# Performance work log

Hardware: AMD Instinct MI355X
Metric: run time of the kernel (lower is better)

## Reference

```python
import jax, jax.numpy as jnp
import numpy as np

N_ENTITY = 100000
N_RELATION = 32
DIM = 64
N_LAYER = 2
B = 4096
T = 64


def setup_inputs() -> dict:
    key = jax.random.key(0)
    ks = jax.random.split(key, 12)
    inp = {
        "items": jax.random.randint(ks[0], (B,), 0, N_ENTITY),
        "user_h": jax.random.randint(ks[1], (N_LAYER, B, T), 0, N_ENTITY),
        "user_r": jax.random.randint(ks[2], (N_LAYER, B, T), 0, N_RELATION),
        "user_t": jax.random.randint(ks[3], (N_LAYER, B, T), 0, N_ENTITY),
        "item_h": jax.random.randint(ks[4], (N_LAYER, B, T), 0, N_ENTITY),
        "item_r": jax.random.randint(ks[5], (N_LAYER, B, T), 0, N_RELATION),
        "item_t": jax.random.randint(ks[6], (N_LAYER, B, T), 0, N_ENTITY),
        # parameters (xavier-ish scale)
        "entity_emb": jax.random.normal(ks[7], (N_ENTITY, DIM), jnp.float32) * 0.05,
        "relation_emb": jax.random.normal(ks[8], (N_RELATION, DIM), jnp.float32) * 0.05,
        # torch Linear(in,out,bias=False) stored here as [in, out] so y = x @ W
        "W1": jax.random.normal(ks[9], (2 * DIM, DIM), jnp.float32) * 0.1,
        "W2": jax.random.normal(ks[10], (DIM, DIM), jnp.float32) * 0.1,
        "W3": jax.random.normal(ks[11], (DIM, 1), jnp.float32) * 0.1,
    }
    return inp


def reference(items, user_h, user_r, user_t, item_h, item_r, item_t,
              entity_emb, relation_emb, W1, W2, W3):
    def knowledge_attention(h_idx, r_idx, t_idx):
        h = entity_emb[h_idx]        # [B, T, d]
        r = relation_emb[r_idx]      # [B, T, d]
        t = entity_emb[t_idx]        # [B, T, d]
        x = jnp.concatenate([h, r], axis=-1)           # [B, T, 2d]
        a = jax.nn.relu(x @ W1)                        # [B, T, d]
        a = jax.nn.relu(a @ W2)                        # [B, T, d]
        a = jax.nn.sigmoid(jnp.squeeze(a @ W3, -1))    # [B, T]
        w = jax.nn.softmax(a, axis=-1)                 # softmax over triples
        return jnp.sum(w[..., None] * t, axis=1)       # [B, d]

    # user embeddings: origin = mean of hop-0 heads, then attention per layer; agg='sum'
    e_u = jnp.mean(entity_emb[user_h[0]], axis=1)
    for i in range(N_LAYER):
        e_u = e_u + knowledge_attention(user_h[i], user_r[i], user_t[i])

    # item embeddings: origin = item entity emb, attention per layer,
    # plus (agg=='sum', n_layer>0) extra mean of hop-0 heads
    e_v = entity_emb[items]
    for i in range(N_LAYER):
        e_v = e_v + knowledge_attention(item_h[i], item_r[i], item_t[i])
    e_v = e_v + jnp.mean(entity_emb[item_h[0]], axis=1)

    scores = jax.nn.sigmoid(jnp.sum(e_v * e_u, axis=1))  # [B]
    return scores
```

## Files before the change

kernel.cpp:

```cpp
#include <hip/hip_runtime.h>
#include <hip/hip_bf16.h>
#include <cstdint>

#define DEV static __device__ __forceinline__

typedef float        v4f __attribute__((ext_vector_type(4)));
typedef short        v8s __attribute__((ext_vector_type(8)));
typedef unsigned int v4u __attribute__((ext_vector_type(4)));

static constexpr int N_ENT = 100000;
static constexpr int BATCH = 4096;

DEV unsigned short f2bf(float f) {
    unsigned int u = __float_as_uint(f);
    u += 0x7fffu + ((u >> 16) & 1u);
    return (unsigned short)(u >> 16);
}
DEV float bflo(unsigned int w) { return __uint_as_float(w << 16); }
DEV float bfhi(unsigned int w) { return __uint_as_float(w & 0xffff0000u); }

__global__ void k0_prep(const float* __restrict__ rel, const float* __restrict__ W1,
                        const float* __restrict__ W2,
                        unsigned short* __restrict__ R1b, unsigned short* __restrict__ W2p,
                        unsigned short* __restrict__ W1p)
{
    const int gid = blockIdx.x * 256 + threadIdx.x;
    if (gid < 2048) {
        const int r = gid >> 6, j = gid & 63;
        float acc = 0.f;
        #pragma unroll 8
        for (int k = 0; k < 64; ++k)
            acc += rel[r * 64 + k] * W1[(64 + k) * 64 + j];
        R1b[gid] = f2bf(acc);
    } else if (gid < 2048 + 4096) {
        const int f = gid - 2048;
        const int i = f & 7, l = (f >> 3) & 63;
        const int tn = (f >> 9) & 3, kk = f >> 11;
        W2p[f] = f2bf(W2[(32 * kk + 8 * (l >> 4) + i) * 64 + 16 * tn + (l & 15)]);
    } else if (gid < 2048 + 8192) {
        const int f = gid - 6144;
        const int i = f & 7, l = (f >> 3) & 63;
        const int tn = (f >> 9) & 3, kk = f >> 11;
        W1p[f] = f2bf(W1[(32 * kk + 8 * (l >> 4) + i) * 64 + 16 * tn + (l & 15)]);
    }
}

__global__ void __launch_bounds__(256) k1_e1(const float* __restrict__ emb,
                                             const unsigned short* __restrict__ W1p,
                                             unsigned short* __restrict__ E1,
                                             unsigned short* __restrict__ E0)
{
    const int lane = threadIdx.x & 63;
    const int q = lane & 15, g = lane >> 4;
    const int wid = blockIdx.x * 4 + (threadIdx.x >> 6);
    const int e0 = wid * 16;
    if (e0 >= N_ENT) return;

    v8s af[2];
    #pragma unroll
    for (int kk = 0; kk < 2; ++kk) {
        const float* p = emb + (size_t)(e0 + q) * 64 + 32 * kk + 8 * g;
        const v4f x = *(const v4f*)p;
        const v4f y = *(const v4f*)(p + 4);
        v8s a;
        a[0] = (short)f2bf(x[0]); a[1] = (short)f2bf(x[1]);
        a[2] = (short)f2bf(x[2]); a[3] = (short)f2bf(x[3]);
        a[4] = (short)f2bf(y[0]); a[5] = (short)f2bf(y[1]);
        a[6] = (short)f2bf(y[2]); a[7] = (short)f2bf(y[3]);
        af[kk] = a;
        v4u pk;
        pk[0] = (unsigned short)a[0] | ((unsigned)(unsigned short)a[1] << 16);
        pk[1] = (unsigned short)a[2] | ((unsigned)(unsigned short)a[3] << 16);
        pk[2] = (unsigned short)a[4] | ((unsigned)(unsigned short)a[5] << 16);
        pk[3] = (unsigned short)a[6] | ((unsigned)(unsigned short)a[7] << 16);
        *(v4u*)(E0 + (size_t)(e0 + q) * 64 + 32 * kk + 8 * g) = pk;
    }

    v4f acc[4];
    #pragma unroll
    for (int tn = 0; tn < 4; ++tn) acc[tn] = (v4f){0.f, 0.f, 0.f, 0.f};
    #pragma unroll
    for (int kk = 0; kk < 2; ++kk)
        #pragma unroll
        for (int tn = 0; tn < 4; ++tn) {
            const v8s bfr = *(const v8s*)(W1p + ((kk * 4 + tn) * 64 + lane) * 8);
            acc[tn] = __builtin_amdgcn_mfma_f32_16x16x32_bf16(af[kk], bfr, acc[tn], 0, 0, 0);
        }
    #pragma unroll
    for (int tn = 0; tn < 4; ++tn)
        #pragma unroll
        for (int i = 0; i < 4; ++i)
            E1[(size_t)(e0 + 4 * g + i) * 64 + 16 * tn + q] = f2bf(acc[tn][i]);
}

__global__ void __launch_bounds__(256, 2) k2_fused(
    const int* __restrict__ items,
    const int* __restrict__ user_h, const int* __restrict__ user_r, const int* __restrict__ user_t,
    const int* __restrict__ item_h, const int* __restrict__ item_r, const int* __restrict__ item_t,
    const float* __restrict__ emb, const unsigned short* __restrict__ E0,
    const unsigned short* __restrict__ E1,
    const unsigned short* __restrict__ R1b, const unsigned short* __restrict__ W2p,
    const float* __restrict__ W3, float* __restrict__ out)
{
    __shared__ float ws_w[4][64];
    __shared__ float att_s[4][64];
    __shared__ float mp[4][64];

    const int lane  = threadIdx.x & 63;
    const int b     = blockIdx.x;
    const int combo = threadIdx.x >> 6;
    const int layer = combo & 1;
    const int side  = combo >> 1, half = combo & 1;
    const int* Hp; const int* Rp; const int* Tp;
    if (combo < 2) { Hp = user_h; Rp = user_r; Tp = user_t; }
    else           { Hp = item_h; Rp = item_r; Tp = item_t; }
    const int base = (layer * BATCH + b) * 64;
    const int* H0p = (side ? item_h : user_h) + b * 64;

    const int q = lane & 15, g = lane >> 4;
    const int sub = lane & 7, grp = lane >> 3;

    int hidx[4], ridx[4];
    #pragma unroll
    for (int tm = 0; tm < 4; ++tm) {
        hidx[tm] = Hp[base + 16 * tm + q];
        ridx[tm] = Rp[base + 16 * tm + q];
    }
    const int tv = Tp[base + lane];
    int midx[4];
    #pragma unroll
    for (int it = 0; it < 4; ++it) midx[it] = H0p[32 * half + 8 * it + grp];

    v4u ev[4][2], rv[4][2];
    #pragma unroll
    for (int tm = 0; tm < 4; ++tm)
        #pragma unroll
        for (int kk = 0; kk < 2; ++kk) {
            ev[tm][kk] = *(const v4u*)(E1  + (size_t)hidx[tm] * 64 + 32 * kk + 8 * g);
            rv[tm][kk] = *(const v4u*)(R1b + (size_t)ridx[tm] * 64 + 32 * kk + 8 * g);
        }
    v4u e0v[8];
    #pragma unroll
    for (int it = 0; it < 8; ++it) {
        const int tr = __shfl(tv, 8 * it + grp);
        e0v[it] = *(const v4u*)(E0 + (size_t)tr * 64 + sub * 8);
    }
    v4u m0v[4];
    #pragma unroll
    for (int it = 0; it < 4; ++it)
        m0v[it] = *(const v4u*)(E0 + (size_t)midx[it] * 64 + sub * 8);

    float w3v[4];
    #pragma unroll
    for (int tn = 0; tn < 4; ++tn) w3v[tn] = W3[16 * tn + q];

    float p[4][4];
    #pragma unroll
    for (int tm = 0; tm < 4; ++tm) {
        v4f a4[4];
        #pragma unroll
        for (int tn = 0; tn < 4; ++tn) a4[tn] = (v4f){0.f, 0.f, 0.f, 0.f};
        #pragma unroll
        for (int kk = 0; kk < 2; ++kk) {
            v8s af;
            #pragma unroll
            for (int w = 0; w < 4; ++w) {
                const unsigned int e = ev[tm][kk][w], r = rv[tm][kk][w];
                af[2 * w]     = (short)f2bf(fmaxf(bflo(e) + bflo(r), 0.f));
                af[2 * w + 1] = (short)f2bf(fmaxf(bfhi(e) + bfhi(r), 0.f));
            }
            #pragma unroll
            for (int tn = 0; tn < 4; ++tn) {
                const v8s bfr = *(const v8s*)(W2p + ((kk * 4 + tn) * 64 + lane) * 8);
                a4[tn] = __builtin_amdgcn_mfma_f32_16x16x32_bf16(af, bfr, a4[tn], 0, 0, 0);
            }
        }
        #pragma unroll
        for (int i = 0; i < 4; ++i) {
            float s = 0.f;
            #pragma unroll
            for (int tn = 0; tn < 4; ++tn)
                s += fmaxf(a4[tn][i], 0.f) * w3v[tn];
            p[tm][i] = s;
        }
    }
    #pragma unroll
    for (int m = 1; m <= 8; m <<= 1)
        #pragma unroll
        for (int tm = 0; tm < 4; ++tm)
            #pragma unroll
            for (int i = 0; i < 4; ++i)
                p[tm][i] += __shfl_xor(p[tm][i], m);

    float ee[4][4];
    float sloc = 0.f;
    #pragma unroll
    for (int tm = 0; tm < 4; ++tm)
        #pragma unroll
        for (int i = 0; i < 4; ++i) {
            const float sg = 1.f / (1.f + __expf(-p[tm][i]));
            const float ex = __expf(sg);
            ee[tm][i] = ex;
            sloc += ex;
        }
    sloc += __shfl_xor(sloc, 16);
    sloc += __shfl_xor(sloc, 32);
    const float rS = 1.f / sloc;

    if (q == 0) {
        #pragma unroll
        for (int tm = 0; tm < 4; ++tm)
            #pragma unroll
            for (int i = 0; i < 4; ++i)
                ws_w[combo][16 * tm + 4 * g + i] = ee[tm][i] * rS;
    }
    __syncthreads();

    float a8[8], m8[8];
    #pragma unroll
    for (int k = 0; k < 8; ++k) { a8[k] = 0.f; m8[k] = 0.f; }
    #pragma unroll
    for (int it = 0; it < 8; ++it) {
        const float w = ws_w[combo][8 * it + grp];
        const v4u e = e0v[it];
        a8[0] += w * bflo(e[0]); a8[1] += w * bfhi(e[0]);
        a8[2] += w * bflo(e[1]); a8[3] += w * bfhi(e[1]);
        a8[4] += w * bflo(e[2]); a8[5] += w * bfhi(e[2]);
        a8[6] += w * bflo(e[3]); a8[7] += w * bfhi(e[3]);
    }
    #pragma unroll
    for (int it = 0; it < 4; ++it) {
        const v4u e = m0v[it];
        m8[0] += bflo(e[0]); m8[1] += bfhi(e[0]);
        m8[2] += bflo(e[1]); m8[3] += bfhi(e[1]);
        m8[4] += bflo(e[2]); m8[5] += bfhi(e[2]);
        m8[6] += bflo(e[3]); m8[7] += bfhi(e[3]);
    }
    #pragma unroll
    for (int m = 8; m <= 32; m <<= 1)
        #pragma unroll
        for (int k = 0; k < 8; ++k) {
            a8[k] += __shfl_xor(a8[k], m);
            m8[k] += __shfl_xor(m8[k], m);
        }
    if (lane < 8) {
        #pragma unroll
        for (int k = 0; k < 8; ++k) {
            att_s[combo][lane * 8 + k] = a8[k];
            mp[combo][lane * 8 + k]    = m8[k];
        }
    }
    __syncthreads();

    if (threadIdx.x < 64) {
        const int j = lane;
        const float eu = att_s[0][j] + att_s[1][j] + (mp[0][j] + mp[1][j]) * (1.f / 64.f);
        const float evv = emb[(size_t)items[b] * 64 + j] + att_s[2][j] + att_s[3][j]
                        + (mp[2][j] + mp[3][j]) * (1.f / 64.f);
        float d = eu * evv;
        #pragma unroll
        for (int m = 1; m <= 32; m <<= 1) d += __shfl_xor(d, m);
        if (lane == 0) out[b] = 1.f / (1.f + __expf(-d));
    }
}

extern "C" void kernel_launch(void* const* d_in, const int* in_sizes, int n_in,
                              void* d_out, int out_size, void* d_ws, size_t ws_size,
                              hipStream_t stream)
{
    const int*   items  = (const int*)d_in[0];
    const int*   user_h = (const int*)d_in[1];
    const int*   user_r = (const int*)d_in[2];
    const int*   user_t = (const int*)d_in[3];
    const int*   item_h = (const int*)d_in[4];
    const int*   item_r = (const int*)d_in[5];
    const int*   item_t = (const int*)d_in[6];
    const float* emb    = (const float*)d_in[7];
    const float* rel    = (const float*)d_in[8];
    const float* W1     = (const float*)d_in[9];
    const float* W2     = (const float*)d_in[10];
    const float* W3     = (const float*)d_in[11];
    float* out = (float*)d_out;

    char* ws = (char*)d_ws;
    const size_t tb = (size_t)N_ENT * 64 * 2;
    unsigned short* E0  = (unsigned short*)ws;
    unsigned short* E1  = (unsigned short*)(ws + tb);
    unsigned short* R1b = (unsigned short*)(ws + 2 * tb);
    unsigned short* W2p = (unsigned short*)(ws + 2 * tb + 4096);
    unsigned short* W1p = (unsigned short*)(ws + 2 * tb + 4096 + 8192);

    hipLaunchKernelGGL(k0_prep, dim3(40), dim3(256), 0, stream, rel, W1, W2, R1b, W2p, W1p);
    hipLaunchKernelGGL(k1_e1, dim3((6250 + 3) / 4), dim3(256), 0, stream, emb, W1p, E1, E0);
    hipLaunchKernelGGL(k2_fused, dim3(BATCH), dim3(256), 0, stream,
                       items, user_h, user_r, user_t, item_h, item_r, item_t,
                       emb, E0, E1, R1b, W2p, W3, out);
}
```

Measured before the change: 76.97 us.

## Raise k2 occupancy, hoist item embedding load, and vectorize bf16 packing and accumulation

Raises the fused kernel's launch bounds from 2 to 4 blocks per CU. The item embedding load is hoisted to the start of the kernel so its latency overlaps other work, and asm barriers pin the gathered loads early. bf16 conversion now goes through the HIP intrinsic with pairwise packing, the attention-weighted sums use packed 2-wide float math, and softmax weights are stored to LDS as vector writes. The higher occupancy target may force register spills, and the intrinsic's rounding of special values may differ slightly from the old manual rounding.

```diff
diff --git a/kernel.cpp b/kernel.cpp
--- a/kernel.cpp
+++ b/kernel.cpp
@@ -5,6 +5,7 @@
 #define DEV static __device__ __forceinline__
 
 typedef float        v4f __attribute__((ext_vector_type(4)));
+typedef float        v2f __attribute__((ext_vector_type(2)));
 typedef short        v8s __attribute__((ext_vector_type(8)));
 typedef unsigned int v4u __attribute__((ext_vector_type(4)));
 
@@ -12,12 +13,15 @@
 static constexpr int BATCH = 4096;
 
 DEV unsigned short f2bf(float f) {
-    unsigned int u = __float_as_uint(f);
-    u += 0x7fffu + ((u >> 16) & 1u);
-    return (unsigned short)(u >> 16);
+    __hip_bfloat16 h = __float2bfloat16(f);
+    return __builtin_bit_cast(unsigned short, h);
+}
+DEV unsigned int pkbf(float lo, float hi) {
+    return (unsigned)f2bf(lo) | ((unsigned)f2bf(hi) << 16);
 }
 DEV float bflo(unsigned int w) { return __uint_as_float(w << 16); }
 DEV float bfhi(unsigned int w) { return __uint_as_float(w & 0xffff0000u); }
+DEV v2f up2(unsigned int w) { return (v2f){bflo(w), bfhi(w)}; }
 
 __global__ void k0_prep(const float* __restrict__ rel, const float* __restrict__ W1,
                         const float* __restrict__ W2,
@@ -62,17 +66,10 @@
         const float* p = emb + (size_t)(e0 + q) * 64 + 32 * kk + 8 * g;
         const v4f x = *(const v4f*)p;
         const v4f y = *(const v4f*)(p + 4);
-        v8s a;
-        a[0] = (short)f2bf(x[0]); a[1] = (short)f2bf(x[1]);
-        a[2] = (short)f2bf(x[2]); a[3] = (short)f2bf(x[3]);
-        a[4] = (short)f2bf(y[0]); a[5] = (short)f2bf(y[1]);
-        a[6] = (short)f2bf(y[2]); a[7] = (short)f2bf(y[3]);
-        af[kk] = a;
         v4u pk;
-        pk[0] = (unsigned short)a[0] | ((unsigned)(unsigned short)a[1] << 16);
-        pk[1] = (unsigned short)a[2] | ((unsigned)(unsigned short)a[3] << 16);
-        pk[2] = (unsigned short)a[4] | ((unsigned)(unsigned short)a[5] << 16);
-        pk[3] = (unsigned short)a[6] | ((unsigned)(unsigned short)a[7] << 16);
+        pk[0] = pkbf(x[0], x[1]); pk[1] = pkbf(x[2], x[3]);
+        pk[2] = pkbf(y[0], y[1]); pk[3] = pkbf(y[2], y[3]);
+        af[kk] = __builtin_bit_cast(v8s, pk);
         *(v4u*)(E0 + (size_t)(e0 + q) * 64 + 32 * kk + 8 * g) = pk;
     }
 
@@ -93,7 +90,7 @@
             E1[(size_t)(e0 + 4 * g + i) * 64 + 16 * tn + q] = f2bf(acc[tn][i]);
 }
 
-__global__ void __launch_bounds__(256, 2) k2_fused(
+__global__ void __launch_bounds__(256, 4) k2_fused(
     const int* __restrict__ items,
     const int* __restrict__ user_h, const int* __restrict__ user_r, const int* __restrict__ user_t,
     const int* __restrict__ item_h, const int* __restrict__ item_r, const int* __restrict__ item_t,
@@ -149,6 +146,13 @@
     #pragma unroll
     for (int it = 0; it < 4; ++it)
         m0v[it] = *(const v4u*)(E0 + (size_t)midx[it] * 64 + sub * 8);
+    float itemv = (combo == 0) ? emb[(size_t)items[b] * 64 + lane] : 0.f;
+
+    #pragma unroll
+    for (int it = 0; it < 8; ++it) asm volatile("" : "+v"(e0v[it]));
+    #pragma unroll
+    for (int it = 0; it < 4; ++it) asm volatile("" : "+v"(m0v[it]));
+    asm volatile("" : "+v"(itemv));
 
     float w3v[4];
     #pragma unroll
@@ -162,13 +166,14 @@
         for (int tn = 0; tn < 4; ++tn) a4[tn] = (v4f){0.f, 0.f, 0.f, 0.f};
         #pragma unroll
         for (int kk = 0; kk < 2; ++kk) {
-            v8s af;
+            v4u afu;
             #pragma unroll
             for (int w = 0; w < 4; ++w) {
                 const unsigned int e = ev[tm][kk][w], r = rv[tm][kk][w];
-                af[2 * w]     = (short)f2bf(fmaxf(bflo(e) + bflo(r), 0.f));
-                af[2 * w + 1] = (short)f2bf(fmaxf(bfhi(e) + bfhi(r), 0.f));
+                afu[w] = pkbf(fmaxf(bflo(e) + bflo(r), 0.f),
+                              fmaxf(bfhi(e) + bfhi(r), 0.f));
             }
+            const v8s af = __builtin_bit_cast(v8s, afu);
             #pragma unroll
             for (int tn = 0; tn < 4; ++tn) {
                 const v8s bfr = *(const v8s*)(W2p + ((kk * 4 + tn) * 64 + lane) * 8);
@@ -209,45 +214,48 @@
 
     if (q == 0) {
         #pragma unroll
-        for (int tm = 0; tm < 4; ++tm)
-            #pragma unroll
-            for (int i = 0; i < 4; ++i)
-                ws_w[combo][16 * tm + 4 * g + i] = ee[tm][i] * rS;
+        for (int tm = 0; tm < 4; ++tm) {
+            v4f wv;
+            #pragma unroll
+            for (int i = 0; i < 4; ++i) wv[i] = ee[tm][i] * rS;
+            *(v4f*)&ws_w[combo][16 * tm + 4 * g] = wv;
+        }
     }
     __syncthreads();
 
-    float a8[8], m8[8];
-    #pragma unroll
-    for (int k = 0; k < 8; ++k) { a8[k] = 0.f; m8[k] = 0.f; }
+    v2f a2[4], m2[4];
+    #pragma unroll
+    for (int c = 0; c < 4; ++c) { a2[c] = (v2f){0.f, 0.f}; m2[c] = (v2f){0.f, 0.f}; }
     #pragma unroll
     for (int it = 0; it < 8; ++it) {
         const float w = ws_w[combo][8 * it + grp];
+        const v2f wv = (v2f){w, w};
         const v4u e = e0v[it];
-        a8[0] += w * bflo(e[0]); a8[1] += w * bfhi(e[0]);
-        a8[2] += w * bflo(e[1]); a8[3] += w * bfhi(e[1]);
-        a8[4] += w * bflo(e[2]); a8[5] += w * bfhi(e[2]);
-        a8[6] += w * bflo(e[3]); a8[7] += w * bfhi(e[3]);
+        #pragma unroll
+        for (int c = 0; c < 4; ++c) a2[c] += wv * up2(e[c]);
     }
     #pragma unroll
     for (int it = 0; it < 4; ++it) {
         const v4u e = m0v[it];
-        m8[0] += bflo(e[0]); m8[1] += bfhi(e[0]);
-        m8[2] += bflo(e[1]); m8[3] += bfhi(e[1]);
-        m8[4] += bflo(e[2]); m8[5] += bfhi(e[2]);
-        m8[6] += bflo(e[3]); m8[7] += bfhi(e[3]);
+        #pragma unroll
+        for (int c = 0; c < 4; ++c) m2[c] += up2(e[c]);
     }
     #pragma unroll
     for (int m = 8; m <= 32; m <<= 1)
         #pragma unroll
-        for (int k = 0; k < 8; ++k) {
-            a8[k] += __shfl_xor(a8[k], m);
-            m8[k] += __shfl_xor(m8[k], m);
+        for (int c = 0; c < 4; ++c) {
+            a2[c][0] += __shfl_xor(a2[c][0], m);
+            a2[c][1] += __shfl_xor(a2[c][1], m);
+            m2[c][0] += __shfl_xor(m2[c][0], m);
+            m2[c][1] += __shfl_xor(m2[c][1], m);
         }
     if (lane < 8) {
         #pragma unroll
-        for (int k = 0; k < 8; ++k) {
-            att_s[combo][lane * 8 + k] = a8[k];
-            mp[combo][lane * 8 + k]    = m8[k];
+        for (int c = 0; c < 4; ++c) {
+            att_s[combo][lane * 8 + 2 * c]     = a2[c][0];
+            att_s[combo][lane * 8 + 2 * c + 1] = a2[c][1];
+            mp[combo][lane * 8 + 2 * c]        = m2[c][0];
+            mp[combo][lane * 8 + 2 * c + 1]    = m2[c][1];
         }
     }
     __syncthreads();
@@ -255,7 +263,7 @@
     if (threadIdx.x < 64) {
         const int j = lane;
         const float eu = att_s[0][j] + att_s[1][j] + (mp[0][j] + mp[1][j]) * (1.f / 64.f);
-        const float evv = emb[(size_t)items[b] * 64 + j] + att_s[2][j] + att_s[3][j]
+        const float evv = itemv + att_s[2][j] + att_s[3][j]
                         + (mp[2][j] + mp[3][j]) * (1.f / 64.f);
         float d = eu * evv;
         #pragma unroll
```

Result: slower. 118.5 us (+54.0%).
